# Performance work log

Hardware: AMD Instinct MI355X
Metric: run time of the kernel (lower is better)

## Reference

```python
import jax, jax.numpy as jnp
import numpy as np

DN = ('NCHW', 'OIHW', 'NCHW')

def dw_conv(x, w, pad):
    # depthwise conv, w: [C,1,k,k], groups=C
    return jax.lax.conv_general_dilated(x, w, (1, 1), [(pad, pad), (pad, pad)],
                                         dimension_numbers=DN, feature_group_count=x.shape[1])

def pw_conv(x, w):
    # 1x1 pointwise conv, w: [Cout,Cin,1,1]
    return jax.lax.conv_general_dilated(x, w, (1, 1), 'VALID', dimension_numbers=DN)

def hardswish(x):
    return x * jnp.clip(x + 3.0, 0.0, 6.0) * (1.0 / 6.0)

def batchnorm(x, g, b, m, v, eps=1e-5):
    scale = (g / jnp.sqrt(v + eps))[None, :, None, None]
    return (x - m[None, :, None, None]) * scale + b[None, :, None, None]

def layernorm(x, g, b, eps=1e-5):
    mu = x.mean(-1, keepdims=True)
    var = x.var(-1, keepdims=True)
    return (x - mu) / jnp.sqrt(var + eps) * g + b

def setup_inputs() -> dict:
    key = jax.random.key(0)
    ks = jax.random.split(key, 16)
    B, C, H, W = 8, 256, 64, 64
    sd = 64   # seg_dim
    s = 0.05  # weight init scale
    inp = {
        'x':   jax.random.normal(ks[0], (B, C, H, W), jnp.float32),
        'seg': jax.random.normal(ks[1], (B, C, H, W), jnp.float32),
        'kv_w':   jax.random.normal(ks[2], (2 * C, C), jnp.float32) * s,
        'q_w':    jax.random.normal(ks[3], (C, C), jnp.float32) * s,
        'proj_w': jax.random.normal(ks[4], (C, C), jnp.float32) * s,
        'proj_b': jnp.zeros((C,), jnp.float32),
        'agg0_dw': jax.random.normal(ks[5], (3 * sd, 1, 3, 3), jnp.float32) * s,
        'agg0_pw': jax.random.normal(ks[6], (sd, 3 * sd, 1, 1), jnp.float32) * s,
        'ln_g': jnp.ones((sd,), jnp.float32), 'ln_b': jnp.zeros((sd,), jnp.float32),
        'agg1_dw': jax.random.normal(ks[7], (sd, 1, 3, 3), jnp.float32) * s,
        'agg1_pw': jax.random.normal(ks[8], (sd, sd, 1, 1), jnp.float32) * s,
        'bn1_g': jnp.ones((sd,), jnp.float32), 'bn1_b': jnp.zeros((sd,), jnp.float32),
        'bn1_m': jnp.zeros((sd,), jnp.float32), 'bn1_v': jnp.ones((sd,), jnp.float32),
        'agg2_dw': jax.random.normal(ks[9], (sd, 1, 5, 5), jnp.float32) * s,
        'agg2_pw': jax.random.normal(ks[10], (sd, sd, 1, 1), jnp.float32) * s,
        'bn2_g': jnp.ones((sd,), jnp.float32), 'bn2_b': jnp.zeros((sd,), jnp.float32),
        'bn2_m': jnp.zeros((sd,), jnp.float32), 'bn2_v': jnp.ones((sd,), jnp.float32),
        'agg3_dw': jax.random.normal(ks[11], (sd, 1, 7, 7), jnp.float32) * s,
        'agg3_pw': jax.random.normal(ks[12], (sd, sd, 1, 1), jnp.float32) * s,
        'bn3_g': jnp.ones((sd,), jnp.float32), 'bn3_b': jnp.zeros((sd,), jnp.float32),
        'bn3_m': jnp.zeros((sd,), jnp.float32), 'bn3_v': jnp.ones((sd,), jnp.float32),
        'crpe_w3': jax.random.normal(ks[13], (48, 1, 3, 3), jnp.float32) * s,
        'crpe_b3': jnp.zeros((48,), jnp.float32),
        'crpe_w5': jax.random.normal(ks[14], (72, 1, 5, 5), jnp.float32) * s,
        'crpe_b5': jnp.zeros((72,), jnp.float32),
        'crpe_w7': jax.random.normal(ks[15], (72, 1, 7, 7), jnp.float32) * s,
        'crpe_b7': jnp.zeros((72,), jnp.float32),
    }
    return inp

def reference(x, seg, kv_w, q_w, proj_w, proj_b, agg0_dw, agg0_pw, ln_g, ln_b,
              agg1_dw, agg1_pw, bn1_g, bn1_b, bn1_m, bn1_v,
              agg2_dw, agg2_pw, bn2_g, bn2_b, bn2_m, bn2_v,
              agg3_dw, agg3_pw, bn3_g, bn3_b, bn3_m, bn3_v,
              crpe_w3, crpe_b3, crpe_w5, crpe_b5, crpe_w7, crpe_b7):
    B, C, H, W = x.shape
    N = H * W
    num_heads = 8
    scale = (C // num_heads) ** -0.5  # head_dim = 32 -> 32^-0.5
    sd = C // 4                       # seg_dim = 64
    Ct = C // 4 * 3                   # trans_dim = 192
    Ch = Ct // num_heads              # 24

    # NOTE: faithful to torch: plain reshape of [B,C,H,W] -> [B,N,C] (no transpose)
    xf = x.reshape(B, N, C)
    sf = seg.reshape(B, N, C)

    kv = (xf @ kv_w.T).reshape(B, N, 2, C)
    kv = jnp.transpose(kv, (2, 0, 1, 3)).reshape(2 * B, N, C)
    q = sf @ q_w.T                                  # [B,N,C]
    qkv = jnp.concatenate([q, kv], axis=0)          # [3B,N,C]

    # ---- Aggregator ----
    xa = jnp.transpose(qkv, (0, 2, 1)).reshape(3 * B, C, H, W)
    c0, c1, c2, c3 = (xa[:, :sd], xa[:, sd:2 * sd], xa[:, 2 * sd:3 * sd], xa[:, 3 * sd:])
    # agg0 branch (local): regroup q/k/v copies into channels
    xl = c3.reshape(3, B, sd, H, W)
    xl = jnp.transpose(xl, (1, 0, 2, 3, 4)).reshape(B, 3 * sd, H, W)
    xl = pw_conv(dw_conv(xl, agg0_dw, 1), agg0_pw)  # [B,sd,H,W]
    xl = jnp.transpose(xl.reshape(B, sd, N), (0, 2, 1))
    x_agg0 = hardswish(layernorm(xl, ln_g, ln_b))   # [B,N,sd]

    x1 = hardswish(batchnorm(pw_conv(dw_conv(c0, agg1_dw, 1), agg1_pw), bn1_g, bn1_b, bn1_m, bn1_v))
    x2 = hardswish(batchnorm(pw_conv(dw_conv(c1, agg2_dw, 2), agg2_pw), bn2_g, bn2_b, bn2_m, bn2_v))
    x3 = hardswish(batchnorm(pw_conv(dw_conv(c2, agg3_dw, 3), agg3_pw), bn3_g, bn3_b, bn3_m, bn3_v))
    xc = jnp.concatenate([x1, x2, x3], axis=1)       # [3B,Ct,H,W]
    qkv_t = xc.reshape(3, B, num_heads, Ch, N)
    qkv_t = jnp.transpose(qkv_t, (0, 1, 2, 4, 3))    # [3,B,h,N,Ch]
    qh, kh, vh = qkv_t[0], qkv_t[1], qkv_t[2]

    # ---- linear attention: softmax over tokens on k, then k^T v ----
    k_sm = jax.nn.softmax(kh, axis=2)                       # softmax over N
    ktv = jnp.einsum('bhnk,bhnv->bhkv', k_sm, vh)           # [B,h,Ch,Ch]
    eff_att = jnp.einsum('bhnk,bhkv->bhnv', qh, ktv)        # [B,h,N,Ch]

    # ---- ConvRelPosEnc ----
    v_img = jnp.transpose(vh, (0, 1, 3, 2)).reshape(B, num_heads * Ch, H, W)
    s1, s2 = 2 * Ch, 2 * Ch + 3 * Ch   # channel splits [48,72,72]
    cv3 = dw_conv(v_img[:, :s1], crpe_w3, 1) + crpe_b3[None, :, None, None]
    cv5 = dw_conv(v_img[:, s1:s2], crpe_w5, 2) + crpe_b5[None, :, None, None]
    cv7 = dw_conv(v_img[:, s2:], crpe_w7, 3) + crpe_b7[None, :, None, None]
    conv_v = jnp.concatenate([cv3, cv5, cv7], axis=1)
    conv_v = jnp.transpose(conv_v.reshape(B, num_heads, Ch, N), (0, 1, 3, 2))  # [B,h,N,Ch]
    crpe = qh * conv_v

    out = scale * eff_att + crpe                     # [B,h,N,Ch]
    out = jnp.transpose(out, (0, 2, 1, 3)).reshape(B, N, Ct)
    out = jnp.concatenate([out, x_agg0], axis=-1)    # [B,N,C]
    out = out @ proj_w.T + proj_b
    return out
```

## Files before the change

kernel.cpp:

```cpp
#include <hip/hip_runtime.h>

#define DI __device__ __forceinline__

typedef unsigned short u16;
typedef __attribute__((ext_vector_type(8))) short bf16x8;
typedef __attribute__((ext_vector_type(8))) unsigned short u16x8;
typedef __attribute__((ext_vector_type(4))) float f32x4;

static constexpr int Cc = 256;
static constexpr int Nn = 4096;

DI float hswish(float v) { return v * fminf(fmaxf(v + 3.f, 0.f), 6.f) * (1.f / 6.f); }

DI u16 f2b(float f) {
  union { float f; unsigned int u; } c; c.f = f;
  return (u16)((c.u + 0x7FFFu + ((c.u >> 16) & 1u)) >> 16);
}
DI float b2f(u16 v) {
  union { unsigned int u; float f; } c; c.u = ((unsigned int)v) << 16; return c.f;
}
DI u16x8 pack8(float4 a, float4 b) {
  u16x8 r;
  r[0] = f2b(a.x); r[1] = f2b(a.y); r[2] = f2b(a.z); r[3] = f2b(a.w);
  r[4] = f2b(b.x); r[5] = f2b(b.y); r[6] = f2b(b.z); r[7] = f2b(b.w);
  return r;
}

typedef const __attribute__((address_space(1))) unsigned int* gas1_t;
typedef __attribute__((address_space(3))) unsigned int* las3_t;
DI void gld16(const void* g, void* l) {
  __builtin_amdgcn_global_load_lds((gas1_t)g, (las3_t)l, 16, 0, 0);
}

__global__ __launch_bounds__(256) void k_qkv(
    const float* __restrict__ x, const float* __restrict__ seg,
    const float* __restrict__ kv_w, const float* __restrict__ q_w,
    u16* __restrict__ qkv)
{
  __shared__ __align__(16) u16 As[2][4096];
  __shared__ __align__(16) u16 Bs[2][4096];
  const int t = threadIdx.x;
  const int lane = t & 63, wave = t >> 6;
  const int n0 = blockIdx.x * 128;
  const int c0 = blockIdx.y * 128;
  const int g  = blockIdx.z;
  const int grp = g >> 3, b = g & 7;
  const float* __restrict__ In = (grp == 0 ? seg : x) + (size_t)b * Nn * Cc;
  const float* __restrict__ Wg = (grp == 0) ? q_w : (kv_w + (grp == 2 ? Cc * Cc : 0));

  const int rA = lane & 15;
  const int kA = (lane >> 4) * 8;
  const int s0 = wave * 2, s1 = wave * 2 + 1;

#define STG(buf, k0)                                                          \
  {                                                                           \
    const float* ap0 = Wg + (size_t)(c0 + s0 * 16 + rA) * Cc + (k0) + kA;     \
    const float* ap1 = Wg + (size_t)(c0 + s1 * 16 + rA) * Cc + (k0) + kA;     \
    const float* bp0 = In + (size_t)(n0 + s0 * 16 + rA) * Cc + (k0) + kA;     \
    const float* bp1 = In + (size_t)(n0 + s1 * 16 + rA) * Cc + (k0) + kA;     \
    float4 a0 = *(const float4*)ap0, a1 = *(const float4*)(ap0 + 4);          \
    float4 a2 = *(const float4*)ap1, a3 = *(const float4*)(ap1 + 4);          \
    float4 b0 = *(const float4*)bp0, b1 = *(const float4*)(bp0 + 4);          \
    float4 b2 = *(const float4*)bp1, b3 = *(const float4*)(bp1 + 4);          \
    *(u16x8*)&As[buf][s0 * 512 + lane * 8] = pack8(a0, a1);                   \
    *(u16x8*)&As[buf][s1 * 512 + lane * 8] = pack8(a2, a3);                   \
    *(u16x8*)&Bs[buf][s0 * 512 + lane * 8] = pack8(b0, b1);                   \
    *(u16x8*)&Bs[buf][s1 * 512 + lane * 8] = pack8(b2, b3);                   \
  }

  f32x4 acc[4][4];
#pragma unroll
  for (int m = 0; m < 4; ++m)
#pragma unroll
    for (int n = 0; n < 4; ++n) acc[m][n] = (f32x4){0.f, 0.f, 0.f, 0.f};

  const int asub = (wave >> 1) * 4;
  const int bsub = (wave & 1) * 4;

  STG(0, 0);
  for (int ks = 0; ks < 8; ++ks) {
    __syncthreads();
    if (ks < 7) STG((ks + 1) & 1, (ks + 1) * 32);
    const int cur = ks & 1;
    bf16x8 af[4], bfr[4];
#pragma unroll
    for (int m = 0; m < 4; ++m)
      af[m] = *(const bf16x8*)&As[cur][(asub + m) * 512 + lane * 8];
#pragma unroll
    for (int n = 0; n < 4; ++n)
      bfr[n] = *(const bf16x8*)&Bs[cur][(bsub + n) * 512 + lane * 8];
#pragma unroll
    for (int m = 0; m < 4; ++m)
#pragma unroll
      for (int n = 0; n < 4; ++n)
        acc[m][n] = __builtin_amdgcn_mfma_f32_16x16x32_bf16(af[m], bfr[n], acc[m][n], 0, 0, 0);
  }
#undef STG

  const int wc = (wave >> 1) * 64, wn = (wave & 1) * 64;
  const int row4 = (lane >> 4) * 4, col = lane & 15;
  u16* __restrict__ op = qkv + (size_t)(g * Cc + c0 + wc) * Nn + n0 + wn;
#pragma unroll
  for (int m = 0; m < 4; ++m)
#pragma unroll
    for (int nn = 0; nn < 4; ++nn)
#pragma unroll
      for (int r = 0; r < 4; ++r)
        op[(size_t)(m * 16 + row4 + r) * Nn + nn * 16 + col] = f2b(acc[m][nn][r]);
}

template <int KS>
DI void dw_plane(const float* __restrict__ sp, const float* __restrict__ wl,
                 u16* __restrict__ dst, float bias, int t)
{
  constexpr int P = KS / 2;
  float wr[KS * KS];
#pragma unroll
  for (int i = 0; i < KS * KS; ++i) wr[i] = wl[i];
  const int x = t & 63;
  const int yb = (t >> 6) << 4;
  float acc[16];
#pragma unroll
  for (int i = 0; i < 16; ++i) acc[i] = bias;
#pragma unroll
  for (int r = 0; r < 16 + 2 * P; ++r) {
    float v[KS];
    const float* rp = sp + (yb + r + (3 - P)) * 72 + x + (4 - P);
#pragma unroll
    for (int dx = 0; dx < KS; ++dx) v[dx] = rp[dx];
#pragma unroll
    for (int dy = 0; dy < KS; ++dy) {
      const int yl = r - dy;
      if (yl >= 0 && yl < 16) {
        float s = acc[yl];
#pragma unroll
        for (int dx = 0; dx < KS; ++dx) s += wr[dy * KS + dx] * v[dx];
        acc[yl] = s;
      }
    }
  }
#pragma unroll
  for (int yl = 0; yl < 16; ++yl) dst[(yb + yl) * 64 + x] = f2b(acc[yl]);
}

DI void dw_stage(const u16* __restrict__ src, float* __restrict__ sp, int t)
{
  for (int i = t; i < 944; i += 256) {
    if (i < 432) {
      int r6 = i / 72, cl = i - r6 * 72;
      int row = (r6 < 3) ? r6 : 64 + r6;
      sp[row * 72 + cl] = 0.f;
    } else {
      int i2 = i - 432;
      int row = 3 + (i2 >> 3), k = i2 & 7;
      int cl = (k < 4) ? k : 64 + k;
      sp[row * 72 + cl] = 0.f;
    }
  }
#pragma unroll
  for (int i = 0; i < 2; ++i) {
    int u = t + i * 256;
    int row = u >> 3, c8 = (u & 7) * 8;
    u16x8 v = *(const u16x8*)(src + row * 64 + c8);
    float4 f0 = make_float4(b2f(v[0]), b2f(v[1]), b2f(v[2]), b2f(v[3]));
    float4 f1 = make_float4(b2f(v[4]), b2f(v[5]), b2f(v[6]), b2f(v[7]));
    *(float4*)&sp[(row + 3) * 72 + 4 + c8] = f0;
    *(float4*)&sp[(row + 3) * 72 + 8 + c8] = f1;
  }
}

__global__ __launch_bounds__(256) void k_dw(
    const u16* __restrict__ qkv,
    const float* __restrict__ a1w, const float* __restrict__ a2w,
    const float* __restrict__ a3w, const float* __restrict__ a0w,
    u16* __restrict__ dwout, u16* __restrict__ dwout0)
{
  __shared__ float sp[70 * 72];
  __shared__ float wl[49];
  const int t = threadIdx.x;
  const int p = blockIdx.x;
  const u16* src; u16* dst; const float* wsp; int ks;
  if (p < 4608) {
    int g = p / 192, c = p % 192, r = c >> 6;
    ks = 3 + 2 * r;
    wsp = (r == 0 ? a1w : (r == 1 ? a2w : a3w)) + (c & 63) * ks * ks;
    src = qkv + (size_t)(g * 256 + c) * Nn;
    dst = dwout + (size_t)p * Nn;
  } else {
    int q = p - 4608;
    int b = q / 192, j = q % 192;
    ks = 3;
    wsp = a0w + j * 9;
    src = qkv + (size_t)(((j >> 6) * 8 + b) * 256 + 192 + (j & 63)) * Nn;
    dst = dwout0 + (size_t)q * Nn;
  }
  if (t < 49) wl[t] = (t < ks * ks) ? wsp[t] : 0.f;
  dw_stage(src, sp, t);
  __syncthreads();
  if (ks == 3)      dw_plane<3>(sp, wl, dst, 0.f, t);
  else if (ks == 5) dw_plane<5>(sp, wl, dst, 0.f, t);
  else              dw_plane<7>(sp, wl, dst, 0.f, t);
}

__global__ __launch_bounds__(256) void k_crpe(
    const u16* __restrict__ xc,
    const float* __restrict__ w3, const float* __restrict__ b3,
    const float* __restrict__ w5, const float* __restrict__ b5,
    const float* __restrict__ w7, const float* __restrict__ b7,
    u16* __restrict__ conv_v)
{
  __shared__ float sp[70 * 72];
  __shared__ float wl[49];
  const int t = threadIdx.x;
  const int p = blockIdx.x;
  const int b = p / 192, ch = p % 192;
  const float* wsp; float bias; int ks;
  if (ch < 48)       { ks = 3; wsp = w3 + ch * 9;          bias = b3[ch]; }
  else if (ch < 120) { ks = 5; wsp = w5 + (ch - 48) * 25;  bias = b5[ch - 48]; }
  else               { ks = 7; wsp = w7 + (ch - 120) * 49; bias = b7[ch - 120]; }
  const u16* src = xc + (size_t)((16 + b) * 192 + ch) * Nn;
  u16* dst = conv_v + (size_t)p * Nn;
  if (t < 49) wl[t] = (t < ks * ks) ? wsp[t] : 0.f;
  dw_stage(src, sp, t);
  __syncthreads();
  if (ks == 3)      dw_plane<3>(sp, wl, dst, bias, t);
  else if (ks == 5) dw_plane<5>(sp, wl, dst, bias, t);
  else              dw_plane<7>(sp, wl, dst, bias, t);
}

__global__ __launch_bounds__(256) void k_pw_bn(
    const u16* __restrict__ dwout,
    const float* __restrict__ w1, const float* __restrict__ w2, const float* __restrict__ w3,
    const float* __restrict__ g1, const float* __restrict__ be1, const float* __restrict__ m1, const float* __restrict__ v1,
    const float* __restrict__ g2, const float* __restrict__ be2, const float* __restrict__ m2, const float* __restrict__ v2,
    const float* __restrict__ g3, const float* __restrict__ be3, const float* __restrict__ m3, const float* __restrict__ v3,
    u16* __restrict__ xc)
{
  constexpr int S2 = 134;
  __shared__ u16 Dl[64 * S2];
  __shared__ __align__(16) u16 Wt[64 * 72];
  __shared__ float scA[64], shA[64];
  const int t = threadIdx.x;
  const int lane = t & 63, wave = t >> 6;
  const int n0 = blockIdx.x * 128;
  const int r = blockIdx.y;
  const int g = blockIdx.z;
  const float* Wp = (r == 0 ? w1 : (r == 1 ? w2 : w3));
  const float* bg = (r == 0 ? g1 : (r == 1 ? g2 : g3));
  const float* bb = (r == 0 ? be1 : (r == 1 ? be2 : be3));
  const float* bm = (r == 0 ? m1 : (r == 1 ? m2 : m3));
  const float* bv = (r == 0 ? v1 : (r == 1 ? v2 : v3));

  {
    int co = t >> 2, ci0 = (t & 3) * 16;
    const float* wp = Wp + co * 64 + ci0;
    float4 w0 = *(const float4*)wp,       wq = *(const float4*)(wp + 4);
    float4 w2_ = *(const float4*)(wp + 8), w3_ = *(const float4*)(wp + 12);
    *(u16x8*)&Wt[co * 72 + ci0] = pack8(w0, wq);
    *(u16x8*)&Wt[co * 72 + ci0 + 8] = pack8(w2_, w3_);
  }
  if (t < 64) {
    float sc = bg[t] * rsqrtf(bv[t] + 1e-5f);
    scA[t] = sc; shA[t] = bb[t] - bm[t] * sc;
  }
  const u16* dbase = dwout + (size_t)(g * 192 + r * 64) * Nn + n0;
#pragma unroll
  for (int i2 = 0; i2 < 4; ++i2) {
    int u = t + i2 * 256;
    int ci = u >> 4, nu = u & 15;
    u16x8 v = *(const u16x8*)(dbase + (size_t)ci * Nn + nu * 8);
    union { u16x8 v; unsigned int w[4]; } cc; cc.v = v;
    int base = ci * S2 + nu * 8;
#pragma unroll
    for (int w = 0; w < 4; ++w) *(unsigned int*)&Dl[base + 2 * w] = cc.w[w];
  }
  __syncthreads();

  f32x4 acc[4][2];
#pragma unroll
  for (int m = 0; m < 4; ++m)
#pragma unroll
    for (int n = 0; n < 2; ++n) acc[m][n] = (f32x4){0.f, 0.f, 0.f, 0.f};

#pragma unroll
  for (int ks = 0; ks < 2; ++ks) {
    const int kbase = ks * 32 + (lane >> 4) * 8;
    bf16x8 af[4];
#pragma unroll
    for (int m = 0; m < 4; ++m)
      af[m] = *(const bf16x8*)&Wt[(m * 16 + (lane & 15)) * 72 + kbase];
#pragma unroll
    for (int nl = 0; nl < 2; ++nl) {
      const int ncol = (wave * 2 + nl) * 16 + (lane & 15);
      bf16x8 bf;
#pragma unroll
      for (int j = 0; j < 8; ++j) bf[j] = (short)Dl[(kbase + j) * S2 + ncol];
#pragma unroll
      for (int m = 0; m < 4; ++m)
        acc[m][nl] = __builtin_amdgcn_mfma_f32_16x16x32_bf16(af[m], bf, acc[m][nl], 0, 0, 0);
    }
  }

  const int row4 = (lane >> 4) * 4, col = lane & 15;
#pragma unroll
  for (int m = 0; m < 4; ++m)
#pragma unroll
    for (int nl = 0; nl < 2; ++nl) {
      int nn = (wave * 2 + nl) * 16 + col;
      u16* op = xc + (size_t)(g * 192 + r * 64 + m * 16 + row4) * Nn + n0 + nn;
#pragma unroll
      for (int rr = 0; rr < 4; ++rr) {
        int co = m * 16 + row4 + rr;
        float v = acc[m][nl][rr] * scA[co] + shA[co];
        op[(size_t)rr * Nn] = f2b(hswish(v));
      }
    }
}

__global__ __launch_bounds__(256) void k_pw_ln(
    const u16* __restrict__ dwout0, const float* __restrict__ pw,
    const float* __restrict__ lng, const float* __restrict__ lnb,
    u16* __restrict__ x_agg0)
{
  constexpr int S2 = 134;
  __shared__ u16 Dl[64 * S2];
  __shared__ __align__(16) u16 Wt[64 * 200];
  __shared__ float lgA[64], lbA[64];
  const int t = threadIdx.x;
  const int lane = t & 63, wave = t >> 6;
  const int n0 = blockIdx.x * 128;
  const int b = blockIdx.y;

#pragma unroll
  for (int i = 0; i < 12; ++i) {
    int u = t + i * 256;
    int co = u / 48, rem = u - co * 48;
    float4 w = *(const float4*)(pw + co * 192 + rem * 4);
    ushort4 o; o.x = f2b(w.x); o.y = f2b(w.y); o.z = f2b(w.z); o.w = f2b(w.w);
    *(ushort4*)&Wt[co * 200 + rem * 4] = o;
  }
  if (t < 64) { lgA[t] = lng[t]; lbA[t] = lnb[t]; }

  f32x4 acc[4][2];
#pragma unroll
  for (int m = 0; m < 4; ++m)
#pragma unroll
    for (int n = 0; n < 2; ++n) acc[m][n] = (f32x4){0.f, 0.f, 0.f, 0.f};

  for (int kc = 0; kc < 192; kc += 64) {
    if (kc) __syncthreads();
    const u16* dbase = dwout0 + (size_t)(b * 192 + kc) * Nn + n0;
#pragma unroll
    for (int i2 = 0; i2 < 4; ++i2) {
      int u = t + i2 * 256;
      int ci = u >> 4, nu = u & 15;
      u16x8 v = *(const u16x8*)(dbase + (size_t)ci * Nn + nu * 8);
      union { u16x8 v; unsigned int w[4]; } cc; cc.v = v;
      int base = ci * S2 + nu * 8;
#pragma unroll
      for (int w = 0; w < 4; ++w) *(unsigned int*)&Dl[base + 2 * w] = cc.w[w];
    }
    __syncthreads();
#pragma unroll
    for (int ks = 0; ks < 2; ++ks) {
      const int kbase = ks * 32 + (lane >> 4) * 8;
      bf16x8 af[4];
#pragma unroll
      for (int m = 0; m < 4; ++m)
        af[m] = *(const bf16x8*)&Wt[(m * 16 + (lane & 15)) * 200 + kc + kbase];
#pragma unroll
      for (int nl = 0; nl < 2; ++nl) {
        const int ncol = (wave * 2 + nl) * 16 + (lane & 15);
        bf16x8 bf;
#pragma unroll
        for (int j = 0; j < 8; ++j) bf[j] = (short)Dl[(kbase + j) * S2 + ncol];
#pragma unroll
        for (int m = 0; m < 4; ++m)
          acc[m][nl] = __builtin_amdgcn_mfma_f32_16x16x32_bf16(af[m], bf, acc[m][nl], 0, 0, 0);
      }
    }
  }

  const int row4 = (lane >> 4) * 4, col = lane & 15;
#pragma unroll
  for (int nl = 0; nl < 2; ++nl) {
    float s = 0.f, q = 0.f;
#pragma unroll
    for (int m = 0; m < 4; ++m)
#pragma unroll
      for (int rr = 0; rr < 4; ++rr) {
        float v = acc[m][nl][rr];
        s += v; q += v * v;
      }
    s += __shfl_xor(s, 16, 64); q += __shfl_xor(q, 16, 64);
    s += __shfl_xor(s, 32, 64); q += __shfl_xor(q, 32, 64);
    float mu = s * (1.f / 64.f);
    float var = q * (1.f / 64.f) - mu * mu;
    float is = rsqrtf(var + 1e-5f);
    int nn = (wave * 2 + nl) * 16 + col;
    u16* op = x_agg0 + (size_t)((b << 12) + n0 + nn) * 64;
#pragma unroll
    for (int m = 0; m < 4; ++m) {
      ushort4 o;
#pragma unroll
      for (int rr = 0; rr < 4; ++rr) {
        int co = m * 16 + row4 + rr;
        float v = (acc[m][nl][rr] - mu) * is * lgA[co] + lbA[co];
        ((u16*)&o)[rr] = f2b(hswish(v));
      }
      *(ushort4*)&op[m * 16 + row4] = o;
    }
  }
}

__global__ __launch_bounds__(256) void k_sm(const u16* __restrict__ xc,
                                            float* __restrict__ ls)
{
  __shared__ float rA[4], rB[4];
  const int rho = blockIdx.x;
  const int b = rho / 192, rem = rho % 192;
  const u16* row = xc + (size_t)((8 + b) * 192 + rem) * Nn;
  const int t = threadIdx.x;
  float v[16];
#pragma unroll
  for (int i = 0; i < 16; ++i) v[i] = b2f(row[t + i * 256]);
  float m = v[0];
#pragma unroll
  for (int i = 1; i < 16; ++i) m = fmaxf(m, v[i]);
#pragma unroll
  for (int off = 32; off > 0; off >>= 1) m = fmaxf(m, __shfl_xor(m, off, 64));
  if ((t & 63) == 0) rA[t >> 6] = m;
  __syncthreads();
  m = fmaxf(fmaxf(rA[0], rA[1]), fmaxf(rA[2], rA[3]));
  float s = 0.f;
#pragma unroll
  for (int i = 0; i < 16; ++i) s += __expf(v[i] - m);
#pragma unroll
  for (int off = 32; off > 0; off >>= 1) s += __shfl_xor(s, off, 64);
  if ((t & 63) == 0) rB[t >> 6] = s;
  __syncthreads();
  if (t == 0) ls[rho] = m + __logf(rB[0] + rB[1] + rB[2] + rB[3]);
}

__global__ __launch_bounds__(576) void k_ktv(const u16* __restrict__ xc,
                                             const float* __restrict__ ls,
                                             float* __restrict__ ktv)
{
  __shared__ float pb[24][65];
  __shared__ float vb[24][65];
  __shared__ float lsl[24];
  const int nc = blockIdx.x, h = blockIdx.y, b = blockIdx.z;
  const int t = threadIdx.x;
  if (t < 24) lsl[t] = ls[(b * 8 + h) * 24 + t];
  __syncthreads();
  const int kk = t / 24, vv = t % 24;
  const u16* kbase = xc + (size_t)((8 + b) * 192 + h * 24) * Nn;
  const u16* vbase = xc + (size_t)((16 + b) * 192 + h * 24) * Nn;
  const int nb0 = nc * 512;
  float accv = 0.f;
  for (int sub = 0; sub < 8; ++sub) {
    int nbase = nb0 + sub * 64;
    for (int e = t; e < 1536; e += 576) {
      int ch = e >> 6, n = e & 63;
      pb[ch][n] = __expf(b2f(kbase[(size_t)ch * Nn + nbase + n]) - lsl[ch]);
      vb[ch][n] = b2f(vbase[(size_t)ch * Nn + nbase + n]);
    }
    __syncthreads();
    float a = 0.f;
#pragma unroll 16
    for (int i = 0; i < 64; ++i) a += pb[kk][i] * vb[vv][i];
    accv += a;
    __syncthreads();
  }
  atomicAdd(&ktv[((b * 8 + h) * 24 + kk) * 24 + vv], accv);
}

__global__ __launch_bounds__(256) void k_cat(
    const u16* __restrict__ xc, const u16* __restrict__ conv_v,
    const float* __restrict__ ktv, const u16* __restrict__ x_agg0,
    u16* __restrict__ catb)
{
  __shared__ float kt[4608];
  const int t = threadIdx.x;
  const int b = blockIdx.y;
  for (int e = t; e < 4608; e += 256) kt[e] = ktv[b * 4608 + e];
  __syncthreads();
  const int nl = t & 63;
  const int grp = t >> 6;
  const int n = blockIdx.x * 64 + nl;
  const float scale = 0.17677669529663687f;
#pragma unroll
  for (int hh = 0; hh < 2; ++hh) {
    const int h = grp * 2 + hh;
    const u16* qb = xc + (size_t)(b * 192 + h * 24) * Nn + n;
    float q[24];
#pragma unroll
    for (int c = 0; c < 24; ++c) q[c] = b2f(qb[(size_t)c * Nn]);
    float ev[24];
#pragma unroll
    for (int v = 0; v < 24; ++v) ev[v] = 0.f;
    const float* kth = kt + h * 576;
#pragma unroll
    for (int k = 0; k < 24; ++k) {
      const float qk = q[k];
#pragma unroll
      for (int v = 0; v < 24; ++v) ev[v] += qk * kth[k * 24 + v];
    }
    const u16* cvb = conv_v + (size_t)(b * 192 + h * 24) * Nn + n;
    u16* ob = catb + ((size_t)(b * 4096 + n)) * 256 + h * 24;
#pragma unroll
    for (int v4 = 0; v4 < 6; ++v4) {
      ushort4 o;
      o.x = f2b(scale * ev[v4 * 4 + 0] + q[v4 * 4 + 0] * b2f(cvb[(size_t)(v4 * 4 + 0) * Nn]));
      o.y = f2b(scale * ev[v4 * 4 + 1] + q[v4 * 4 + 1] * b2f(cvb[(size_t)(v4 * 4 + 1) * Nn]));
      o.z = f2b(scale * ev[v4 * 4 + 2] + q[v4 * 4 + 2] * b2f(cvb[(size_t)(v4 * 4 + 2) * Nn]));
      o.w = f2b(scale * ev[v4 * 4 + 3] + q[v4 * 4 + 3] * b2f(cvb[(size_t)(v4 * 4 + 3) * Nn]));
      *(ushort4*)(ob + v4 * 4) = o;
    }
  }
  const u16* xa = x_agg0 + ((size_t)(b * 4096 + blockIdx.x * 64)) * 64;
  u16* cb = catb + ((size_t)(b * 4096 + blockIdx.x * 64)) * 256 + 192;
  for (int e2 = t; e2 < 4096; e2 += 256) {
    int nn = e2 >> 6, cc = e2 & 63;
    cb[(size_t)nn * 256 + cc] = xa[(size_t)nn * 64 + cc];
  }
}

__global__ __launch_bounds__(256) void k_proj(
    const u16* __restrict__ catb, const float* __restrict__ pwf,
    const float* __restrict__ pb, float* __restrict__ out)
{
  __shared__ __align__(16) u16 As[2][4096];
  __shared__ __align__(16) u16 Bs[2][4096];
  const int t = threadIdx.x;
  const int lane = t & 63, wave = t >> 6;
  const int m0 = blockIdx.x * 128;
  const int c0 = blockIdx.y * 128;
  const int rA = lane & 15;
  const int kA = (lane >> 4) * 8;
  const int s0 = wave * 2, s1 = wave * 2 + 1;

#define STG(buf, k0)                                                          \
  {                                                                           \
    gld16(catb + (size_t)(m0 + s0 * 16 + rA) * 256 + (k0) + kA, &As[buf][s0 * 512]); \
    gld16(catb + (size_t)(m0 + s1 * 16 + rA) * 256 + (k0) + kA, &As[buf][s1 * 512]); \
    const float* bp0 = pwf + (size_t)(c0 + s0 * 16 + rA) * 256 + (k0) + kA;   \
    const float* bp1 = pwf + (size_t)(c0 + s1 * 16 + rA) * 256 + (k0) + kA;   \
    float4 b0 = *(const float4*)bp0, b1 = *(const float4*)(bp0 + 4);          \
    float4 b2 = *(const float4*)bp1, b3 = *(const float4*)(bp1 + 4);          \
    *(u16x8*)&Bs[buf][s0 * 512 + lane * 8] = pack8(b0, b1);                   \
    *(u16x8*)&Bs[buf][s1 * 512 + lane * 8] = pack8(b2, b3);                   \
  }

  f32x4 acc[4][4];
#pragma unroll
  for (int m = 0; m < 4; ++m)
#pragma unroll
    for (int n = 0; n < 4; ++n) acc[m][n] = (f32x4){0.f, 0.f, 0.f, 0.f};

  const int asub = (wave >> 1) * 4;
  const int bsub = (wave & 1) * 4;

  STG(0, 0);
  for (int ks = 0; ks < 8; ++ks) {
    __syncthreads();
    if (ks < 7) STG((ks + 1) & 1, (ks + 1) * 32);
    const int cur = ks & 1;
    bf16x8 af[4], bfr[4];
#pragma unroll
    for (int m = 0; m < 4; ++m)
      af[m] = *(const bf16x8*)&As[cur][(asub + m) * 512 + lane * 8];
#pragma unroll
    for (int n = 0; n < 4; ++n)
      bfr[n] = *(const bf16x8*)&Bs[cur][(bsub + n) * 512 + lane * 8];
#pragma unroll
    for (int m = 0; m < 4; ++m)
#pragma unroll
      for (int n = 0; n < 4; ++n)
        acc[m][n] = __builtin_amdgcn_mfma_f32_16x16x32_bf16(af[m], bfr[n], acc[m][n], 0, 0, 0);
  }
#undef STG

  const int wm = (wave >> 1) * 64, wn = (wave & 1) * 64;
  const int row4 = (lane >> 4) * 4, col = lane & 15;
  float pbv[4];
#pragma unroll
  for (int nn = 0; nn < 4; ++nn) pbv[nn] = pb[c0 + wn + nn * 16 + col];
  float* __restrict__ op = out + (size_t)(m0 + wm) * 256 + c0 + wn;
#pragma unroll
  for (int mi = 0; mi < 4; ++mi)
#pragma unroll
    for (int nn = 0; nn < 4; ++nn)
#pragma unroll
      for (int r = 0; r < 4; ++r)
        op[(size_t)(mi * 16 + row4 + r) * 256 + nn * 16 + col] = acc[mi][nn][r] + pbv[nn];
}

extern "C" void kernel_launch(void* const* d_in, const int* in_sizes, int n_in,
                              void* d_out, int out_size, void* d_ws, size_t ws_size,
                              hipStream_t stream)
{
  const float* x       = (const float*)d_in[0];
  const float* seg     = (const float*)d_in[1];
  const float* kv_w    = (const float*)d_in[2];
  const float* q_w     = (const float*)d_in[3];
  const float* proj_w  = (const float*)d_in[4];
  const float* proj_b  = (const float*)d_in[5];
  const float* agg0_dw = (const float*)d_in[6];
  const float* agg0_pw = (const float*)d_in[7];
  const float* ln_g    = (const float*)d_in[8];
  const float* ln_b    = (const float*)d_in[9];
  const float* agg1_dw = (const float*)d_in[10];
  const float* agg1_pw = (const float*)d_in[11];
  const float* bn1_g   = (const float*)d_in[12];
  const float* bn1_b   = (const float*)d_in[13];
  const float* bn1_m   = (const float*)d_in[14];
  const float* bn1_v   = (const float*)d_in[15];
  const float* agg2_dw = (const float*)d_in[16];
  const float* agg2_pw = (const float*)d_in[17];
  const float* bn2_g   = (const float*)d_in[18];
  const float* bn2_b   = (const float*)d_in[19];
  const float* bn2_m   = (const float*)d_in[20];
  const float* bn2_v   = (const float*)d_in[21];
  const float* agg3_dw = (const float*)d_in[22];
  const float* agg3_pw = (const float*)d_in[23];
  const float* bn3_g   = (const float*)d_in[24];
  const float* bn3_b   = (const float*)d_in[25];
  const float* bn3_m   = (const float*)d_in[26];
  const float* bn3_v   = (const float*)d_in[27];
  const float* crpe_w3 = (const float*)d_in[28];
  const float* crpe_b3 = (const float*)d_in[29];
  const float* crpe_w5 = (const float*)d_in[30];
  const float* crpe_b5 = (const float*)d_in[31];
  const float* crpe_w7 = (const float*)d_in[32];
  const float* crpe_b7 = (const float*)d_in[33];

  float* ws = (float*)d_ws;
  u16*   qkv_b  = (u16*)(ws);
  u16*   dwout  = (u16*)(ws + 12582912);
  u16*   dwout0 = (u16*)(ws + 22020096);
  u16*   xc_b   = (u16*)(ws + 25165824);
  u16*   conv_v = (u16*)(ws + 37748736);
  u16*   x_agg0 = (u16*)(ws + 40894464);
  float* ls     = ws + 41943040;
  float* ktv    = ws + 41944576;
  u16*   catb   = (u16*)(ws + 41981440);
  float* out    = (float*)d_out;

  hipMemsetAsync(ktv, 0, 36864 * sizeof(float), stream);

  k_qkv<<<dim3(32, 2, 24), 256, 0, stream>>>(x, seg, kv_w, q_w, qkv_b);
  k_dw<<<dim3(6144), 256, 0, stream>>>(qkv_b, agg1_dw, agg2_dw, agg3_dw, agg0_dw,
                                       dwout, dwout0);
  k_pw_bn<<<dim3(32, 3, 24), 256, 0, stream>>>(
      dwout, agg1_pw, agg2_pw, agg3_pw,
      bn1_g, bn1_b, bn1_m, bn1_v,
      bn2_g, bn2_b, bn2_m, bn2_v,
      bn3_g, bn3_b, bn3_m, bn3_v, xc_b);
  k_pw_ln<<<dim3(32, 8), 256, 0, stream>>>(dwout0, agg0_pw, ln_g, ln_b, x_agg0);
  k_sm<<<dim3(1536), 256, 0, stream>>>(xc_b, ls);
  k_ktv<<<dim3(8, 8, 8), 576, 0, stream>>>(xc_b, ls, ktv);
  k_crpe<<<dim3(1536), 256, 0, stream>>>(xc_b, crpe_w3, crpe_b3, crpe_w5,
                                         crpe_b5, crpe_w7, crpe_b7, conv_v);
  k_cat<<<dim3(64, 8), 256, 0, stream>>>(xc_b, conv_v, ktv, x_agg0, catb);
  k_proj<<<dim3(256, 2), 256, 0, stream>>>(catb, proj_w, proj_b, out);
}
```

Measured before the change: 363.0 us.

## Register-prefetch GEMM pipelines and fold softmax normalization into ktv accumulation

The qkv and proj GEMMs now prefetch the next two k-slices into registers, write them to LDS, and sync with an explicit lgkmcnt wait plus s_barrier. This replaces the global_load_lds path and the per-iteration __syncthreads, aiming to overlap global latency with MFMA work. The separate softmax-stat kernel is removed: k_ktv accumulates exp(k) together with its column sum Z, and k_cat divides ktv by Z. Dropping the max subtraction risks exp overflow for large k values, and the kernel also drops a barrier and vectorizes its loads.

```diff
diff --git a/kernel.cpp b/kernel.cpp
--- a/kernel.cpp
+++ b/kernel.cpp
@@ -26,11 +26,13 @@
   return r;
 }
 
-typedef const __attribute__((address_space(1))) unsigned int* gas1_t;
-typedef __attribute__((address_space(3))) unsigned int* las3_t;
-DI void gld16(const void* g, void* l) {
-  __builtin_amdgcn_global_load_lds((gas1_t)g, (las3_t)l, 16, 0, 0);
-}
+#define SYNC_PIPE()                                                           \
+  {                                                                           \
+    asm volatile("s_waitcnt lgkmcnt(0)" ::: "memory");                        \
+    __builtin_amdgcn_sched_barrier(0);                                        \
+    __builtin_amdgcn_s_barrier();                                             \
+    __builtin_amdgcn_sched_barrier(0);                                        \
+  }
 
 __global__ __launch_bounds__(256) void k_qkv(
     const float* __restrict__ x, const float* __restrict__ seg,
@@ -51,21 +53,26 @@
   const int rA = lane & 15;
   const int kA = (lane >> 4) * 8;
   const int s0 = wave * 2, s1 = wave * 2 + 1;
-
-#define STG(buf, k0)                                                          \
+  const float* __restrict__ ap0 = Wg + (size_t)(c0 + s0 * 16 + rA) * Cc + kA;
+  const float* __restrict__ ap1 = Wg + (size_t)(c0 + s1 * 16 + rA) * Cc + kA;
+  const float* __restrict__ bp0 = In + (size_t)(n0 + s0 * 16 + rA) * Cc + kA;
+  const float* __restrict__ bp1 = In + (size_t)(n0 + s1 * 16 + rA) * Cc + kA;
+
+  float4 Ra[8], Rb[8];
+
+#define LOADS(R, k0)                                                          \
   {                                                                           \
-    const float* ap0 = Wg + (size_t)(c0 + s0 * 16 + rA) * Cc + (k0) + kA;     \
-    const float* ap1 = Wg + (size_t)(c0 + s1 * 16 + rA) * Cc + (k0) + kA;     \
-    const float* bp0 = In + (size_t)(n0 + s0 * 16 + rA) * Cc + (k0) + kA;     \
-    const float* bp1 = In + (size_t)(n0 + s1 * 16 + rA) * Cc + (k0) + kA;     \
-    float4 a0 = *(const float4*)ap0, a1 = *(const float4*)(ap0 + 4);          \
-    float4 a2 = *(const float4*)ap1, a3 = *(const float4*)(ap1 + 4);          \
-    float4 b0 = *(const float4*)bp0, b1 = *(const float4*)(bp0 + 4);          \
-    float4 b2 = *(const float4*)bp1, b3 = *(const float4*)(bp1 + 4);          \
-    *(u16x8*)&As[buf][s0 * 512 + lane * 8] = pack8(a0, a1);                   \
-    *(u16x8*)&As[buf][s1 * 512 + lane * 8] = pack8(a2, a3);                   \
-    *(u16x8*)&Bs[buf][s0 * 512 + lane * 8] = pack8(b0, b1);                   \
-    *(u16x8*)&Bs[buf][s1 * 512 + lane * 8] = pack8(b2, b3);                   \
+    R[0] = *(const float4*)(ap0 + (k0)); R[1] = *(const float4*)(ap0 + (k0) + 4); \
+    R[2] = *(const float4*)(ap1 + (k0)); R[3] = *(const float4*)(ap1 + (k0) + 4); \
+    R[4] = *(const float4*)(bp0 + (k0)); R[5] = *(const float4*)(bp0 + (k0) + 4); \
+    R[6] = *(const float4*)(bp1 + (k0)); R[7] = *(const float4*)(bp1 + (k0) + 4); \
+  }
+#define WRITES(R, buf)                                                        \
+  {                                                                           \
+    *(u16x8*)&As[buf][s0 * 512 + lane * 8] = pack8(R[0], R[1]);               \
+    *(u16x8*)&As[buf][s1 * 512 + lane * 8] = pack8(R[2], R[3]);               \
+    *(u16x8*)&Bs[buf][s0 * 512 + lane * 8] = pack8(R[4], R[5]);               \
+    *(u16x8*)&Bs[buf][s1 * 512 + lane * 8] = pack8(R[6], R[7]);               \
   }
 
   f32x4 acc[4][4];
@@ -77,25 +84,38 @@
   const int asub = (wave >> 1) * 4;
   const int bsub = (wave & 1) * 4;
 
-  STG(0, 0);
-  for (int ks = 0; ks < 8; ++ks) {
-    __syncthreads();
-    if (ks < 7) STG((ks + 1) & 1, (ks + 1) * 32);
-    const int cur = ks & 1;
-    bf16x8 af[4], bfr[4];
-#pragma unroll
-    for (int m = 0; m < 4; ++m)
-      af[m] = *(const bf16x8*)&As[cur][(asub + m) * 512 + lane * 8];
-#pragma unroll
-    for (int n = 0; n < 4; ++n)
-      bfr[n] = *(const bf16x8*)&Bs[cur][(bsub + n) * 512 + lane * 8];
-#pragma unroll
-    for (int m = 0; m < 4; ++m)
-#pragma unroll
-      for (int n = 0; n < 4; ++n)
-        acc[m][n] = __builtin_amdgcn_mfma_f32_16x16x32_bf16(af[m], bfr[n], acc[m][n], 0, 0, 0);
-  }
-#undef STG
+#define COMPUTE(cur)                                                          \
+  {                                                                           \
+    bf16x8 af[4], bfr[4];                                                     \
+    _Pragma("unroll")                                                         \
+    for (int m = 0; m < 4; ++m)                                               \
+      af[m] = *(const bf16x8*)&As[cur][(asub + m) * 512 + lane * 8];          \
+    _Pragma("unroll")                                                         \
+    for (int n = 0; n < 4; ++n)                                               \
+      bfr[n] = *(const bf16x8*)&Bs[cur][(bsub + n) * 512 + lane * 8];         \
+    _Pragma("unroll")                                                         \
+    for (int m = 0; m < 4; ++m)                                               \
+      _Pragma("unroll")                                                       \
+      for (int n = 0; n < 4; ++n)                                             \
+        acc[m][n] = __builtin_amdgcn_mfma_f32_16x16x32_bf16(af[m], bfr[n], acc[m][n], 0, 0, 0); \
+  }
+
+  LOADS(Ra, 0);
+  LOADS(Rb, 32);
+#pragma unroll
+  for (int kk = 0; kk < 4; ++kk) {
+    WRITES(Ra, 0);
+    if (kk < 3) LOADS(Ra, (kk * 2 + 2) * 32);
+    SYNC_PIPE();
+    COMPUTE(0);
+    WRITES(Rb, 1);
+    if (kk < 3) LOADS(Rb, (kk * 2 + 3) * 32);
+    SYNC_PIPE();
+    COMPUTE(1);
+  }
+#undef LOADS
+#undef WRITES
+#undef COMPUTE
 
   const int wc = (wave >> 1) * 64, wn = (wave & 1) * 64;
   const int row4 = (lane >> 4) * 4, col = lane & 15;
@@ -413,77 +433,59 @@
   }
 }
 
-__global__ __launch_bounds__(256) void k_sm(const u16* __restrict__ xc,
-                                            float* __restrict__ ls)
-{
-  __shared__ float rA[4], rB[4];
-  const int rho = blockIdx.x;
-  const int b = rho / 192, rem = rho % 192;
-  const u16* row = xc + (size_t)((8 + b) * 192 + rem) * Nn;
-  const int t = threadIdx.x;
-  float v[16];
-#pragma unroll
-  for (int i = 0; i < 16; ++i) v[i] = b2f(row[t + i * 256]);
-  float m = v[0];
-#pragma unroll
-  for (int i = 1; i < 16; ++i) m = fmaxf(m, v[i]);
-#pragma unroll
-  for (int off = 32; off > 0; off >>= 1) m = fmaxf(m, __shfl_xor(m, off, 64));
-  if ((t & 63) == 0) rA[t >> 6] = m;
-  __syncthreads();
-  m = fmaxf(fmaxf(rA[0], rA[1]), fmaxf(rA[2], rA[3]));
-  float s = 0.f;
-#pragma unroll
-  for (int i = 0; i < 16; ++i) s += __expf(v[i] - m);
-#pragma unroll
-  for (int off = 32; off > 0; off >>= 1) s += __shfl_xor(s, off, 64);
-  if ((t & 63) == 0) rB[t >> 6] = s;
-  __syncthreads();
-  if (t == 0) ls[rho] = m + __logf(rB[0] + rB[1] + rB[2] + rB[3]);
-}
-
 __global__ __launch_bounds__(576) void k_ktv(const u16* __restrict__ xc,
-                                             const float* __restrict__ ls,
-                                             float* __restrict__ ktv)
+                                             float* __restrict__ ktv,
+                                             float* __restrict__ Z)
 {
   __shared__ float pb[24][65];
   __shared__ float vb[24][65];
-  __shared__ float lsl[24];
   const int nc = blockIdx.x, h = blockIdx.y, b = blockIdx.z;
   const int t = threadIdx.x;
-  if (t < 24) lsl[t] = ls[(b * 8 + h) * 24 + t];
-  __syncthreads();
-  const int kk = t / 24, vv = t % 24;
+  const int kk = t / 24, vv = t - kk * 24;
   const u16* kbase = xc + (size_t)((8 + b) * 192 + h * 24) * Nn;
   const u16* vbase = xc + (size_t)((16 + b) * 192 + h * 24) * Nn;
   const int nb0 = nc * 512;
-  float accv = 0.f;
+  float accv = 0.f, accz = 0.f;
   for (int sub = 0; sub < 8; ++sub) {
+    if (sub) __syncthreads();
     int nbase = nb0 + sub * 64;
-    for (int e = t; e < 1536; e += 576) {
-      int ch = e >> 6, n = e & 63;
-      pb[ch][n] = __expf(b2f(kbase[(size_t)ch * Nn + nbase + n]) - lsl[ch]);
-      vb[ch][n] = b2f(vbase[(size_t)ch * Nn + nbase + n]);
+    if (t < 384) {
+      int which = t >= 192;
+      int i = which ? t - 192 : t;
+      int ch = i >> 3, c8 = (i & 7) * 8;
+      const u16* sp = (which ? vbase : kbase) + (size_t)ch * Nn + nbase + c8;
+      u16x8 v = *(const u16x8*)sp;
+      float* dst = which ? &vb[ch][c8] : &pb[ch][c8];
+      if (!which) {
+#pragma unroll
+        for (int j = 0; j < 8; ++j) dst[j] = __expf(b2f(v[j]));
+      } else {
+#pragma unroll
+        for (int j = 0; j < 8; ++j) dst[j] = b2f(v[j]);
+      }
     }
     __syncthreads();
-    float a = 0.f;
+    float a = 0.f, z = 0.f;
 #pragma unroll 16
-    for (int i = 0; i < 64; ++i) a += pb[kk][i] * vb[vv][i];
-    accv += a;
-    __syncthreads();
+    for (int i = 0; i < 64; ++i) { float p = pb[kk][i]; a += p * vb[vv][i]; z += p; }
+    accv += a; accz += z;
   }
   atomicAdd(&ktv[((b * 8 + h) * 24 + kk) * 24 + vv], accv);
+  if (vv == 0) atomicAdd(&Z[(b * 8 + h) * 24 + kk], accz);
 }
 
 __global__ __launch_bounds__(256) void k_cat(
     const u16* __restrict__ xc, const u16* __restrict__ conv_v,
-    const float* __restrict__ ktv, const u16* __restrict__ x_agg0,
-    u16* __restrict__ catb)
+    const float* __restrict__ ktv, const float* __restrict__ Z,
+    const u16* __restrict__ x_agg0, u16* __restrict__ catb)
 {
   __shared__ float kt[4608];
   const int t = threadIdx.x;
   const int b = blockIdx.y;
-  for (int e = t; e < 4608; e += 256) kt[e] = ktv[b * 4608 + e];
+  for (int e = t; e < 4608; e += 256) {
+    int h = e / 576, rem = e - h * 576, k = rem / 24;
+    kt[e] = ktv[b * 4608 + e] / Z[b * 192 + h * 24 + k];
+  }
   __syncthreads();
   const int nl = t & 63;
   const int grp = t >> 6;
@@ -539,17 +541,27 @@
   const int rA = lane & 15;
   const int kA = (lane >> 4) * 8;
   const int s0 = wave * 2, s1 = wave * 2 + 1;
-
-#define STG(buf, k0)                                                          \
+  const u16*   __restrict__ aq0 = catb + (size_t)(m0 + s0 * 16 + rA) * 256 + kA;
+  const u16*   __restrict__ aq1 = catb + (size_t)(m0 + s1 * 16 + rA) * 256 + kA;
+  const float* __restrict__ bp0 = pwf + (size_t)(c0 + s0 * 16 + rA) * 256 + kA;
+  const float* __restrict__ bp1 = pwf + (size_t)(c0 + s1 * 16 + rA) * 256 + kA;
+
+  u16x8 Ua[2], Ub[2];
+  float4 Fa[4], Fb[4];
+
+#define LOADS(U, F, k0)                                                       \
   {                                                                           \
-    gld16(catb + (size_t)(m0 + s0 * 16 + rA) * 256 + (k0) + kA, &As[buf][s0 * 512]); \
-    gld16(catb + (size_t)(m0 + s1 * 16 + rA) * 256 + (k0) + kA, &As[buf][s1 * 512]); \
-    const float* bp0 = pwf + (size_t)(c0 + s0 * 16 + rA) * 256 + (k0) + kA;   \
-    const float* bp1 = pwf + (size_t)(c0 + s1 * 16 + rA) * 256 + (k0) + kA;   \
-    float4 b0 = *(const float4*)bp0, b1 = *(const float4*)(bp0 + 4);          \
-    float4 b2 = *(const float4*)bp1, b3 = *(const float4*)(bp1 + 4);          \
-    *(u16x8*)&Bs[buf][s0 * 512 + lane * 8] = pack8(b0, b1);                   \
-    *(u16x8*)&Bs[buf][s1 * 512 + lane * 8] = pack8(b2, b3);                   \
+    U[0] = *(const u16x8*)(aq0 + (k0));                                       \
+    U[1] = *(const u16x8*)(aq1 + (k0));                                       \
+    F[0] = *(const float4*)(bp0 + (k0)); F[1] = *(const float4*)(bp0 + (k0) + 4); \
+    F[2] = *(const float4*)(bp1 + (k0)); F[3] = *(const float4*)(bp1 + (k0) + 4); \
+  }
+#define WRITES(U, F, buf)                                                     \
+  {                                                                           \
+    *(u16x8*)&As[buf][s0 * 512 + lane * 8] = U[0];                            \
+    *(u16x8*)&As[buf][s1 * 512 + lane * 8] = U[1];                            \
+    *(u16x8*)&Bs[buf][s0 * 512 + lane * 8] = pack8(F[0], F[1]);               \
+    *(u16x8*)&Bs[buf][s1 * 512 + lane * 8] = pack8(F[2], F[3]);               \
   }
 
   f32x4 acc[4][4];
@@ -561,25 +573,38 @@
   const int asub = (wave >> 1) * 4;
   const int bsub = (wave & 1) * 4;
 
-  STG(0, 0);
-  for (int ks = 0; ks < 8; ++ks) {
-    __syncthreads();
-    if (ks < 7) STG((ks + 1) & 1, (ks + 1) * 32);
-    const int cur = ks & 1;
-    bf16x8 af[4], bfr[4];
-#pragma unroll
-    for (int m = 0; m < 4; ++m)
-      af[m] = *(const bf16x8*)&As[cur][(asub + m) * 512 + lane * 8];
-#pragma unroll
-    for (int n = 0; n < 4; ++n)
-      bfr[n] = *(const bf16x8*)&Bs[cur][(bsub + n) * 512 + lane * 8];
-#pragma unroll
-    for (int m = 0; m < 4; ++m)
-#pragma unroll
-      for (int n = 0; n < 4; ++n)
-        acc[m][n] = __builtin_amdgcn_mfma_f32_16x16x32_bf16(af[m], bfr[n], acc[m][n], 0, 0, 0);
-  }
-#undef STG
+#define COMPUTE(cur)                                                          \
+  {                                                                           \
+    bf16x8 af[4], bfr[4];                                                     \
+    _Pragma("unroll")                                                         \
+    for (int m = 0; m < 4; ++m)                                               \
+      af[m] = *(const bf16x8*)&As[cur][(asub + m) * 512 + lane * 8];          \
+    _Pragma("unroll")                                                         \
+    for (int n = 0; n < 4; ++n)                                               \
+      bfr[n] = *(const bf16x8*)&Bs[cur][(bsub + n) * 512 + lane * 8];         \
+    _Pragma("unroll")                                                         \
+    for (int m = 0; m < 4; ++m)                                               \
+      _Pragma("unroll")                                                       \
+      for (int n = 0; n < 4; ++n)                                             \
+        acc[m][n] = __builtin_amdgcn_mfma_f32_16x16x32_bf16(af[m], bfr[n], acc[m][n], 0, 0, 0); \
+  }
+
+  LOADS(Ua, Fa, 0);
+  LOADS(Ub, Fb, 32);
+#pragma unroll
+  for (int kk = 0; kk < 4; ++kk) {
+    WRITES(Ua, Fa, 0);
+    if (kk < 3) LOADS(Ua, Fa, (kk * 2 + 2) * 32);
+    SYNC_PIPE();
+    COMPUTE(0);
+    WRITES(Ub, Fb, 1);
+    if (kk < 3) LOADS(Ub, Fb, (kk * 2 + 3) * 32);
+    SYNC_PIPE();
+    COMPUTE(1);
+  }
+#undef LOADS
+#undef WRITES
+#undef COMPUTE
 
   const int wm = (wave >> 1) * 64, wn = (wave & 1) * 64;
   const int row4 = (lane >> 4) * 4, col = lane & 15;
@@ -642,12 +667,12 @@
   u16*   xc_b   = (u16*)(ws + 25165824);
   u16*   conv_v = (u16*)(ws + 37748736);
   u16*   x_agg0 = (u16*)(ws + 40894464);
-  float* ls     = ws + 41943040;
+  float* Z      = ws + 41943040;
   float* ktv    = ws + 41944576;
   u16*   catb   = (u16*)(ws + 41981440);
   float* out    = (float*)d_out;
 
-  hipMemsetAsync(ktv, 0, 36864 * sizeof(float), stream);
+  hipMemsetAsync(Z, 0, (1536 + 36864) * sizeof(float), stream);
 
   k_qkv<<<dim3(32, 2, 24), 256, 0, stream>>>(x, seg, kv_w, q_w, qkv_b);
   k_dw<<<dim3(6144), 256, 0, stream>>>(qkv_b, agg1_dw, agg2_dw, agg3_dw, agg0_dw,
@@ -658,10 +683,9 @@
       bn2_g, bn2_b, bn2_m, bn2_v,
       bn3_g, bn3_b, bn3_m, bn3_v, xc_b);
   k_pw_ln<<<dim3(32, 8), 256, 0, stream>>>(dwout0, agg0_pw, ln_g, ln_b, x_agg0);
-  k_sm<<<dim3(1536), 256, 0, stream>>>(xc_b, ls);
-  k_ktv<<<dim3(8, 8, 8), 576, 0, stream>>>(xc_b, ls, ktv);
+  k_ktv<<<dim3(8, 8, 8), 576, 0, stream>>>(xc_b, ktv, Z);
   k_crpe<<<dim3(1536), 256, 0, stream>>>(xc_b, crpe_w3, crpe_b3, crpe_w5,
                                          crpe_b5, crpe_w7, crpe_b7, conv_v);
-  k_cat<<<dim3(64, 8), 256, 0, stream>>>(xc_b, conv_v, ktv, x_agg0, catb);
+  k_cat<<<dim3(64, 8), 256, 0, stream>>>(xc_b, conv_v, ktv, Z, x_agg0, catb);
   k_proj<<<dim3(256, 2), 256, 0, stream>>>(catb, proj_w, proj_b, out);
 }
```

Result: slower. 393.3 us (+8.3%).
